# Kernel optimization log

Measured on AMD Instinct MI355X. Metric: run time of the kernel, lower is better.

## Reference

```python
import jax, jax.numpy as jnp
import numpy as np

V, D, DI, DS, DC, DTR, L, H, BS, B, T = 32000, 512, 1024, 16, 4, 32, 4, 2048, 1024, 2, 1024


def layer_norm(x, g, b):
    m = jnp.mean(x, axis=-1, keepdims=True)
    v = jnp.mean(jnp.square(x - m), axis=-1, keepdims=True)
    return (x - m) * jax.lax.rsqrt(v + 1e-5) * g + b


def mamba(x, p):
    # x: [B, T, D]
    Bb = x.shape[0]
    xz = jnp.einsum('btd,ed->bte', x, p['W_in'])          # [B,T,2*DI]
    u, z = jnp.split(xz, 2, axis=-1)
    # causal depthwise conv over time
    uc = jnp.transpose(u, (0, 2, 1))                       # [B,DI,T]
    uc = jax.lax.conv_general_dilated(uc, p['conv_w'][:, None, :], (1,), [(DC - 1, 0)], feature_group_count=DI)
    uc = uc + p['conv_b'][None, :, None]
    u = jax.nn.silu(jnp.transpose(uc, (0, 2, 1)))          # [B,T,DI]
    x_dbl = jnp.einsum('btd,ed->bte', u, p['W_xp'])        # [B,T,DTR+2*DS]
    dt = jax.nn.softplus(jnp.einsum('btr,dr->btd', x_dbl[..., :DTR], p['W_dt']) + p['b_dt'])  # [B,T,DI]
    Bm = x_dbl[..., DTR:DTR + DS]                          # [B,T,DS]
    Cm = x_dbl[..., DTR + DS:]                             # [B,T,DS]
    A = -jnp.exp(p['A_log'])                               # [DI,DS]

    def step(h, inp):
        dt_t, B_t, C_t, u_t = inp                          # [B,DI],[B,DS],[B,DS],[B,DI]
        dA = jnp.exp(dt_t[:, :, None] * A)                 # [B,DI,DS]
        h = dA * h + (dt_t * u_t)[:, :, None] * B_t[:, None, :]
        return h, jnp.einsum('bds,bs->bd', h, C_t)

    h0 = jnp.zeros((Bb, DI, DS), x.dtype)
    _, ys = jax.lax.scan(step, h0, (dt.transpose(1, 0, 2), Bm.transpose(1, 0, 2), Cm.transpose(1, 0, 2), u.transpose(1, 0, 2)))
    y = ys.transpose(1, 0, 2) + u * p['D_p']               # skip term D*u
    y = y * jax.nn.silu(z)
    return jnp.einsum('bte,de->btd', y, p['W_out'])


def setup_inputs() -> dict:
    key = jax.random.key(0)
    ks = jax.random.split(key, 16)
    s = 0.02
    rn = lambda k, sh: (jax.random.normal(k, sh, jnp.float32) * s)
    inp = {
        'idx': jax.random.randint(ks[0], (B, T), 0, V),
        'tok_emb': rn(ks[1], (V, D)),
        'pos_emb': rn(ks[2], (BS, D)),
        'ln1_g': jnp.ones((L, D), jnp.float32), 'ln1_b': jnp.zeros((L, D), jnp.float32),
        'W_in': rn(ks[3], (L, 2 * DI, D)),
        'conv_w': rn(ks[4], (L, DI, DC)), 'conv_b': jnp.zeros((L, DI), jnp.float32),
        'W_xp': rn(ks[5], (L, DTR + 2 * DS, DI)),
        'W_dt': rn(ks[6], (L, DI, DTR)), 'b_dt': jnp.full((L, DI), -4.6, jnp.float32),
        'A_log': jnp.tile(jnp.log(jnp.arange(1, DS + 1, dtype=jnp.float32))[None, None, :], (L, DI, 1)),
        'D_p': jnp.ones((L, DI), jnp.float32),
        'W_out': rn(ks[7], (L, D, DI)),
        'ln2_g': jnp.ones((L, D), jnp.float32), 'ln2_b': jnp.zeros((L, D), jnp.float32),
        'W_f1': rn(ks[8], (L, H, D)), 'b_f1': jnp.zeros((L, H), jnp.float32),
        'W_f2': rn(ks[9], (L, D, H)), 'b_f2': jnp.zeros((L, D), jnp.float32),
        'lm_w': rn(ks[10], (V, D)), 'lm_b': jnp.zeros((V,), jnp.float32),
    }
    return inp


def reference(idx, tok_emb, pos_emb, ln1_g, ln1_b, W_in, conv_w, conv_b, W_xp, W_dt, b_dt, A_log, D_p, W_out, ln2_g, ln2_b, W_f1, b_f1, W_f2, b_f2, lm_w, lm_b):
    x = tok_emb[idx] + pos_emb[:idx.shape[1]]              # [B,T,D]
    layers = {'ln1_g': ln1_g, 'ln1_b': ln1_b, 'W_in': W_in, 'conv_w': conv_w, 'conv_b': conv_b,
              'W_xp': W_xp, 'W_dt': W_dt, 'b_dt': b_dt, 'A_log': A_log, 'D_p': D_p, 'W_out': W_out,
              'ln2_g': ln2_g, 'ln2_b': ln2_b, 'W_f1': W_f1, 'b_f1': b_f1, 'W_f2': W_f2, 'b_f2': b_f2}

    def blk(x, p):
        x = x + mamba(layer_norm(x, p['ln1_g'], p['ln1_b']), p)
        h = layer_norm(x, p['ln2_g'], p['ln2_b'])
        h = jax.nn.relu(jnp.einsum('btd,hd->bth', h, p['W_f1']) + p['b_f1'])
        x = x + jnp.einsum('bth,dh->btd', h, p['W_f2']) + p['b_f2']
        return x, None

    x, _ = jax.lax.scan(blk, x, layers)
    logits = jnp.einsum('btd,vd->btv', x, lm_w) + lm_b     # [B,T,V]
    return logits
```

## Files before the change

### kernel.cpp

```cpp
#include <hip/hip_runtime.h>
#include <cstdint>
#include <cstddef>

typedef __bf16 bf16;
typedef __bf16 bf16x8 __attribute__((ext_vector_type(8)));
typedef __bf16 bf16x4 __attribute__((ext_vector_type(4)));
typedef float  f32x4  __attribute__((ext_vector_type(4)));

#define D_MODEL 512
#define D_INNER 1024
#define D_STATE 16
#define D_CONV  4
#define DT_RANK 32
#define N_LAYER 4
#define H_FFN   2048
#define SEQ_T   1024
#define BATCH   2
#define BT      (BATCH * SEQ_T)
#define VOCAB   32000

#define NCHUNK  16
#define CHUNK   (SEQ_T / NCHUNK)

#define KSPLIT  4

__device__ __forceinline__ float b2f(bf16 x) { return (float)x; }
__device__ __forceinline__ bf16  f2b(float x) { return (bf16)x; }

__device__ __forceinline__ float rdf(const void* p, long i, int bf) {
  return bf ? (float)((const bf16*)p)[i] : ((const float*)p)[i];
}

__device__ __forceinline__ void async16(const void* g, void* l) {
  __builtin_amdgcn_global_load_lds((const __attribute__((address_space(1))) void*)g,
                                   (__attribute__((address_space(3))) void*)l, 16, 0, 0);
}

__global__ void probe_k(const unsigned short* __restrict__ tok,
                        const unsigned short* __restrict__ pos,
                        int* __restrict__ flag)
{
  int lane = threadIdx.x;
  int bad = 0;
  for (int i = lane; i < 512; i += 64) {
    int e0 = (tok[i] >> 7) & 0xFF;
    int e1 = (pos[i] >> 7) & 0xFF;
    if (e0 >= 134 || e1 >= 134) bad = 1;
  }
  unsigned long long m = __ballot(bad);
  if (lane == 0) *flag = (m == 0ULL) ? 1 : 0;
}

__global__ __launch_bounds__(256) void cvt_k(const float4* __restrict__ src,
                                             bf16* __restrict__ dst,
                                             int n4, const int* __restrict__ dflag)
{
  if (*dflag) return;
  int i = blockIdx.x * 256 + threadIdx.x;
  if (i >= n4) return;
  float4 v = src[i];
  bf16x4 o; o[0] = f2b(v.x); o[1] = f2b(v.y); o[2] = f2b(v.z); o[3] = f2b(v.w);
  *(bf16x4*)(dst + (size_t)i * 4) = o;
}

template<int OUTMODE, bool RELU, bool SWZ>
__global__ __launch_bounds__(256) void gemm_nt(
    const bf16* __restrict__ A, const bf16* __restrict__ Barena,
    const void* __restrict__ Braw, long boff,
    void* __restrict__ Cout, const void* __restrict__ bias, long biasoff,
    const float* __restrict__ res, const int* __restrict__ dflag,
    int M, int N, int K, int ldc, int col0)
{
  __shared__ __attribute__((aligned(16))) bf16 As[128 * 32];
  __shared__ __attribute__((aligned(16))) bf16 Bs[128 * 32];

  const int bf = *dflag;
  const bf16* Bw = bf ? ((const bf16*)Braw + boff) : Barena;

  const int tid  = threadIdx.x;
  const int lane = tid & 63;
  const int q    = lane >> 4;
  const int m16  = lane & 15;
  const int w    = tid >> 6;
  const int wr   = w >> 1, wc = w & 1;

  int bx = blockIdx.x, by = blockIdx.y;
  if (SWZ) {
    int gx = gridDim.x, gy = gridDim.y;
    int n  = gx * gy;
    if ((n & 7) == 0) {
      int id  = by * gx + bx;
      int nid = (id & 7) * (n >> 3) + (id >> 3);
      bx = nid / gy;
      by = nid % gy;
    }
  }

  const int rowA0 = by * 128;
  const int rowB0 = bx * 128;

  f32x4 acc[4][4] = {};

  for (int k0 = 0; k0 < K; k0 += 32) {
#pragma unroll
    for (int r = 0; r < 2; r++) {
      int ci  = r * 256 + tid;
      int row = ci >> 2;
      int kc  = ci & 3;
      const bf16* ga = A  + (size_t)(rowA0 + row) * K + (k0 + kc * 8);
      const bf16* gb = Bw + (size_t)(rowB0 + row) * K + (k0 + kc * 8);
      char* la = (char*)As + (size_t)(r * 256 + (tid & 192)) * 16;
      char* lb = (char*)Bs + (size_t)(r * 256 + (tid & 192)) * 16;
      async16(ga, la);
      async16(gb, lb);
    }
    __syncthreads();

    bf16x8 af[4], bfr[4];
#pragma unroll
    for (int mt = 0; mt < 4; mt++)
      af[mt] = *(const bf16x8*)&As[(wr * 64 + mt * 16 + m16) * 32 + q * 8];
#pragma unroll
    for (int nt = 0; nt < 4; nt++)
      bfr[nt] = *(const bf16x8*)&Bs[(wc * 64 + nt * 16 + m16) * 32 + q * 8];

#pragma unroll
    for (int mt = 0; mt < 4; mt++)
#pragma unroll
      for (int nt = 0; nt < 4; nt++)
        acc[mt][nt] = __builtin_amdgcn_mfma_f32_16x16x32_bf16(
            af[mt], bfr[nt], acc[mt][nt], 0, 0, 0);

    __syncthreads();
  }

#pragma unroll
  for (int mt = 0; mt < 4; mt++) {
#pragma unroll
    for (int r = 0; r < 4; r++) {
      int row = rowA0 + wr * 64 + mt * 16 + q * 4 + r;
#pragma unroll
      for (int nt = 0; nt < 4; nt++) {
        int col = col0 + rowB0 + wc * 64 + nt * 16 + m16;
        float v = acc[mt][nt][r];
        if (bias) v += rdf(bias, biasoff + col, bf);
        if (res)  v += res[(size_t)row * ldc + col];
        if (RELU) v = fmaxf(v, 0.f);
        size_t oi = (size_t)row * ldc + col;
        if (OUTMODE == 1 || (OUTMODE == 2 && bf)) ((bf16*)Cout)[oi] = f2b(v);
        else                                      ((float*)Cout)[oi] = v;
      }
    }
  }
}

__global__ __launch_bounds__(256) void gemm_nt_sk(
    const bf16* __restrict__ A, const bf16* __restrict__ Barena,
    const void* __restrict__ Braw, long boff,
    float* __restrict__ Cpart, const int* __restrict__ dflag,
    int M, int N, int K)
{
  __shared__ __attribute__((aligned(16))) bf16 As[128 * 32];
  __shared__ __attribute__((aligned(16))) bf16 Bs[128 * 32];

  const int bf = *dflag;
  const bf16* Bw = bf ? ((const bf16*)Braw + boff) : Barena;

  const int tid  = threadIdx.x;
  const int lane = tid & 63;
  const int q    = lane >> 4;
  const int m16  = lane & 15;
  const int w    = tid >> 6;
  const int wr   = w >> 1, wc = w & 1;

  const int rowA0 = blockIdx.y * 128;
  const int rowB0 = blockIdx.x * 128;
  const int ks    = blockIdx.z;
  const int kBeg  = ks * (K / KSPLIT);
  const int kEnd  = kBeg + (K / KSPLIT);

  f32x4 acc[4][4] = {};

  for (int k0 = kBeg; k0 < kEnd; k0 += 32) {
#pragma unroll
    for (int r = 0; r < 2; r++) {
      int ci  = r * 256 + tid;
      int row = ci >> 2;
      int kc  = ci & 3;
      const bf16* ga = A  + (size_t)(rowA0 + row) * K + (k0 + kc * 8);
      const bf16* gb = Bw + (size_t)(rowB0 + row) * K + (k0 + kc * 8);
      char* la = (char*)As + (size_t)(r * 256 + (tid & 192)) * 16;
      char* lb = (char*)Bs + (size_t)(r * 256 + (tid & 192)) * 16;
      async16(ga, la);
      async16(gb, lb);
    }
    __syncthreads();

    bf16x8 af[4], bfr[4];
#pragma unroll
    for (int mt = 0; mt < 4; mt++)
      af[mt] = *(const bf16x8*)&As[(wr * 64 + mt * 16 + m16) * 32 + q * 8];
#pragma unroll
    for (int nt = 0; nt < 4; nt++)
      bfr[nt] = *(const bf16x8*)&Bs[(wc * 64 + nt * 16 + m16) * 32 + q * 8];

#pragma unroll
    for (int mt = 0; mt < 4; mt++)
#pragma unroll
      for (int nt = 0; nt < 4; nt++)
        acc[mt][nt] = __builtin_amdgcn_mfma_f32_16x16x32_bf16(
            af[mt], bfr[nt], acc[mt][nt], 0, 0, 0);

    __syncthreads();
  }

#pragma unroll
  for (int mt = 0; mt < 4; mt++) {
#pragma unroll
    for (int r = 0; r < 4; r++) {
      int row = rowA0 + wr * 64 + mt * 16 + q * 4 + r;
#pragma unroll
      for (int nt = 0; nt < 4; nt++) {
        int col = rowB0 + wc * 64 + nt * 16 + m16;
        Cpart[((size_t)ks * M + row) * N + col] = acc[mt][nt][r];
      }
    }
  }
}

__global__ __launch_bounds__(256) void redk_k(const float* __restrict__ part,
                                              const void* __restrict__ bias, long biasoff,
                                              const float* __restrict__ res,
                                              float* __restrict__ out,
                                              int n, int N, const int* __restrict__ dflag)
{
  int bf = *dflag;
  int i = blockIdx.x * 256 + threadIdx.x;
  if (i >= n) return;
  f32x4 s = ((const f32x4*)part)[i];
#pragma unroll
  for (int ks = 1; ks < KSPLIT; ks++) {
    f32x4 p = ((const f32x4*)part)[(size_t)ks * n + i];
    s.x += p.x; s.y += p.y; s.z += p.z; s.w += p.w;
  }
  if (bias) {
    int col = (i * 4) & (N - 1);
    s.x += rdf(bias, biasoff + col,     bf);
    s.y += rdf(bias, biasoff + col + 1, bf);
    s.z += rdf(bias, biasoff + col + 2, bf);
    s.w += rdf(bias, biasoff + col + 3, bf);
  }
  if (res) {
    f32x4 r = ((const f32x4*)res)[i];
    s.x += r.x; s.y += r.y; s.z += r.z; s.w += r.w;
  }
  ((f32x4*)out)[i] = s;
}

__global__ void embed_k(const int* __restrict__ idx, const void* __restrict__ tok,
                        const void* __restrict__ pos, float* __restrict__ x,
                        const int* __restrict__ dflag)
{
  int bf = *dflag;
  int bt = blockIdx.x;
  int t  = bt & (SEQ_T - 1);
  long rowv = idx[bt];
  for (int i = threadIdx.x; i < D_MODEL; i += blockDim.x)
    x[(size_t)bt * D_MODEL + i] = rdf(tok, rowv * D_MODEL + i, bf)
                                + rdf(pos, (long)t * D_MODEL + i, bf);
}

__global__ __launch_bounds__(64) void ln_k(const float* __restrict__ x,
                                           const void* __restrict__ g,
                                           const void* __restrict__ bb,
                                           long goff,
                                           bf16* __restrict__ out,
                                           const int* __restrict__ dflag)
{
  int bf = *dflag;
  int row = blockIdx.x;
  const float4* xr = (const float4*)(x + (size_t)row * D_MODEL);
  int l = threadIdx.x;
  float4 v0 = xr[l];
  float4 v1 = xr[64 + l];
  float s  = (v0.x + v0.y) + (v0.z + v0.w) + (v1.x + v1.y) + (v1.z + v1.w);
  float ss = v0.x*v0.x + v0.y*v0.y + v0.z*v0.z + v0.w*v0.w
           + v1.x*v1.x + v1.y*v1.y + v1.z*v1.z + v1.w*v1.w;
#pragma unroll
  for (int o = 32; o; o >>= 1) { s += __shfl_xor(s, o); ss += __shfl_xor(ss, o); }
  float m   = s  * (1.f / 512.f);
  float var = ss * (1.f / 512.f) - m * m;
  float inv = rsqrtf(var + 1e-5f);
  float vs[8] = {v0.x, v0.y, v0.z, v0.w, v1.x, v1.y, v1.z, v1.w};
  int i0 = l * 4, i1 = 256 + l * 4;
#pragma unroll
  for (int e = 0; e < 4; e++) {
    out[(size_t)row * D_MODEL + i0 + e] =
        f2b((vs[e] - m) * inv * rdf(g, goff + i0 + e, bf) + rdf(bb, goff + i0 + e, bf));
    out[(size_t)row * D_MODEL + i1 + e] =
        f2b((vs[4 + e] - m) * inv * rdf(g, goff + i1 + e, bf) + rdf(bb, goff + i1 + e, bf));
  }
}

__global__ __launch_bounds__(256) void conv_silu_k(const float* __restrict__ xz,
                                                   const void* __restrict__ cw,
                                                   const void* __restrict__ cb,
                                                   long cwoff, long cboff,
                                                   bf16* __restrict__ u,
                                                   const int* __restrict__ dflag)
{
  int bf  = *dflag;
  int gid = blockIdx.x * 256 + threadIdx.x;
  int d   = gid & (D_INNER - 1);
  int bt  = gid >> 10;
  int t   = bt & (SEQ_T - 1);
  float acc = rdf(cb, cboff + d, bf);
#pragma unroll
  for (int k = 0; k < D_CONV; k++) {
    int tt = t + k - (D_CONV - 1);
    if (tt >= 0)
      acc += xz[(size_t)(bt + k - (D_CONV - 1)) * (2 * D_INNER) + d]
           * rdf(cw, cwoff + (long)d * D_CONV + k, bf);
  }
  float sig = 1.f / (1.f + __expf(-acc));
  u[gid] = f2b(acc * sig);
}

__global__ __launch_bounds__(256) void xdbl_k(const bf16* __restrict__ u,
                                              const bf16* __restrict__ Warena,
                                              const void* __restrict__ Wraw, long woff,
                                              float* __restrict__ xd,
                                              const int* __restrict__ dflag)
{
  int bf = *dflag;
  const bf16* Wxp = bf ? ((const bf16*)Wraw + woff) : Warena;
  int t = blockIdx.x;
  __shared__ float us[D_INNER];
  __shared__ float red[256];
  if (threadIdx.x < D_INNER / 8) {
    bf16x8 v = *(const bf16x8*)(u + (size_t)t * D_INNER + threadIdx.x * 8);
#pragma unroll
    for (int e = 0; e < 8; e++) us[threadIdx.x * 8 + e] = b2f(v[e]);
  }
  __syncthreads();
  int j = threadIdx.x >> 2, p = threadIdx.x & 3;
  const bf16x8* wr = (const bf16x8*)(Wxp + (size_t)j * D_INNER + p * 256);
  float s = 0.f;
#pragma unroll 4
  for (int c = 0; c < 32; c++) {
    bf16x8 wv = wr[c];
    int k = p * 256 + c * 8;
#pragma unroll
    for (int e = 0; e < 8; e++) s += us[k + e] * b2f(wv[e]);
  }
  red[threadIdx.x] = s;
  __syncthreads();
  if (p == 0)
    xd[(size_t)t * 64 + j] = red[threadIdx.x] + red[threadIdx.x + 1]
                           + red[threadIdx.x + 2] + red[threadIdx.x + 3];
}

__global__ __launch_bounds__(256) void dt_k(const float* __restrict__ xd,
                                            const bf16* __restrict__ Warena,
                                            const void* __restrict__ Wraw, long woff,
                                            const void* __restrict__ bdt, long boff,
                                            float* __restrict__ dtb,
                                            const int* __restrict__ dflag)
{
  int bf = *dflag;
  const bf16* Wdt = bf ? ((const bf16*)Wraw + woff) : Warena;
  int t = blockIdx.x >> 2;
  int d = ((blockIdx.x & 3) << 8) + threadIdx.x;
  __shared__ float xr[DT_RANK];
  if (threadIdx.x < DT_RANK) xr[threadIdx.x] = xd[(size_t)t * 64 + threadIdx.x];
  __syncthreads();
  float s = rdf(bdt, boff + d, bf);
  const bf16x8* wr = (const bf16x8*)(Wdt + (size_t)d * DT_RANK);
#pragma unroll
  for (int c = 0; c < 4; c++) {
    bf16x8 wv = wr[c];
#pragma unroll
    for (int e = 0; e < 8; e++) s += xr[c * 8 + e] * b2f(wv[e]);
  }
  s = (s > 20.f) ? s : log1pf(__expf(s));
  dtb[(size_t)t * D_INNER + d] = s;
}

__global__ __launch_bounds__(256) void scanA_k(const float* __restrict__ dtb,
                                               const bf16* __restrict__ u,
                                               const float* __restrict__ xd,
                                               const void* __restrict__ A_log, long aoff,
                                               float* __restrict__ Pb,
                                               float* __restrict__ Qb,
                                               const int* __restrict__ dflag)
{
  int bf = *dflag;
  int s  = threadIdx.x & 15;
  int dl = threadIdx.x >> 4;
  int c  = blockIdx.x & (NCHUNK - 1);
  int dg = (blockIdx.x >> 4) & 63;
  int b  = blockIdx.x >> 10;
  int d  = dg * 16 + dl;

  float Av = -__expf(rdf(A_log, aoff + (long)d * D_STATE + s, bf));
  float h = 0.f, P = 1.f;
  size_t row0 = (size_t)b * SEQ_T + (size_t)c * CHUNK;

  float dt_n = dtb[row0 * D_INNER + d];
  float u_n  = b2f(u[row0 * D_INNER + d]);
  float B_n  = xd[row0 * 64 + DT_RANK + s];

  for (int t = 0; t < CHUNK; t++) {
    float dt_v = dt_n, u_v = u_n, Bv = B_n;
    if (t + 1 < CHUNK) {
      size_t r1 = row0 + t + 1;
      dt_n = dtb[r1 * D_INNER + d];
      u_n  = b2f(u[r1 * D_INNER + d]);
      B_n  = xd[r1 * 64 + DT_RANK + s];
    }
    float dA = __expf(dt_v * Av);
    P *= dA;
    h = dA * h + (dt_v * u_v) * Bv;
  }
  size_t o = (((size_t)b * D_INNER + d) * D_STATE + s) * NCHUNK + c;
  Pb[o] = P;
  Qb[o] = h;
}

__global__ __launch_bounds__(256) void scanB_k(const float* __restrict__ Pb,
                                               const float* __restrict__ Qb,
                                               float* __restrict__ Hin)
{
  int tid = blockIdx.x * 256 + threadIdx.x;
  size_t base = (size_t)tid * NCHUNK;
  float h = 0.f;
#pragma unroll
  for (int c = 0; c < NCHUNK; c++) {
    Hin[base + c] = h;
    h = Pb[base + c] * h + Qb[base + c];
  }
}

__global__ __launch_bounds__(256) void scanC_k(const float* __restrict__ dtb,
                                               const bf16* __restrict__ u,
                                               const float* __restrict__ xd,
                                               const float* __restrict__ xz,
                                               const void* __restrict__ A_log, long aoff,
                                               const void* __restrict__ D_p, long doff,
                                               const float* __restrict__ Hin,
                                               bf16* __restrict__ y,
                                               const int* __restrict__ dflag)
{
  int bf = *dflag;
  int s  = threadIdx.x & 15;
  int dl = threadIdx.x >> 4;
  int c  = blockIdx.x & (NCHUNK - 1);
  int dg = (blockIdx.x >> 4) & 63;
  int b  = blockIdx.x >> 10;
  int d  = dg * 16 + dl;

  float Av = -__expf(rdf(A_log, aoff + (long)d * D_STATE + s, bf));
  float Dv = rdf(D_p, doff + d, bf);
  float h  = Hin[(((size_t)b * D_INNER + d) * D_STATE + s) * NCHUNK + c];
  size_t row0 = (size_t)b * SEQ_T + (size_t)c * CHUNK;

  float dt_n = dtb[row0 * D_INNER + d];
  float u_n  = b2f(u[row0 * D_INNER + d]);
  float B_n  = xd[row0 * 64 + DT_RANK + s];
  float C_n  = xd[row0 * 64 + DT_RANK + D_STATE + s];

  for (int t = 0; t < CHUNK; t++) {
    float dt_v = dt_n, u_v = u_n, Bv = B_n, Cv = C_n;
    if (t + 1 < CHUNK) {
      size_t r1 = row0 + t + 1;
      dt_n = dtb[r1 * D_INNER + d];
      u_n  = b2f(u[r1 * D_INNER + d]);
      B_n  = xd[r1 * 64 + DT_RANK + s];
      C_n  = xd[r1 * 64 + DT_RANK + D_STATE + s];
    }
    float dA = __expf(dt_v * Av);
    h = dA * h + (dt_v * u_v) * Bv;
    float p = h * Cv;
    p += __shfl_xor(p, 1);
    p += __shfl_xor(p, 2);
    p += __shfl_xor(p, 4);
    p += __shfl_xor(p, 8);
    if (s == 0) {
      size_t r = row0 + t;
      float zv  = xz[r * (2 * D_INNER) + D_INNER + d];
      float sig = 1.f / (1.f + __expf(-zv));
      y[r * D_INNER + d] = f2b((p + u_v * Dv) * (zv * sig));
    }
  }
}

__global__ void cast_k(const float* __restrict__ x, bf16* __restrict__ o, int n)
{
  int i = blockIdx.x * 256 + threadIdx.x;
  if (i < n) o[i] = f2b(x[i]);
}

extern "C" void kernel_launch(void* const* d_in, const int* in_sizes, int n_in,
                              void* d_out, int out_size, void* d_ws, size_t ws_size,
                              hipStream_t stream)
{
  const int* idx = (const int*)d_in[0];
  const void* tok    = d_in[1];
  const void* pos    = d_in[2];
  const void* ln1_g  = d_in[3];
  const void* ln1_b  = d_in[4];
  const void* W_in   = d_in[5];
  const void* conv_w = d_in[6];
  const void* conv_b = d_in[7];
  const void* W_xp   = d_in[8];
  const void* W_dt   = d_in[9];
  const void* b_dt   = d_in[10];
  const void* A_log  = d_in[11];
  const void* D_p    = d_in[12];
  const void* W_out  = d_in[13];
  const void* ln2_g  = d_in[14];
  const void* ln2_b  = d_in[15];
  const void* W_f1   = d_in[16];
  const void* b_f1   = d_in[17];
  const void* W_f2   = d_in[18];
  const void* b_f2   = d_in[19];
  const void* lm_w   = d_in[20];
  const void* lm_b   = d_in[21];

  char* ws = (char*)d_ws;
  int*  dflag = (int*)ws;    ws += 256;
  float* x_res = (float*)ws; ws += (size_t)BT * D_MODEL * 4;
  float* xz    = (float*)ws; ws += (size_t)BT * 2 * D_INNER * 4;
  float* xdbl  = (float*)ws; ws += (size_t)BT * 64 * 4;
  float* dtb   = (float*)ws; ws += (size_t)BT * D_INNER * 4;
  bf16* lnbuf  = (bf16*)ws;  ws += (size_t)BT * D_MODEL * 2;
  bf16* ubuf   = (bf16*)ws;  ws += (size_t)BT * D_INNER * 2;
  bf16* ybuf   = (bf16*)ws;  ws += (size_t)BT * D_INNER * 2;
  bf16* hbuf   = (bf16*)ws;  ws += (size_t)BT * H_FFN * 2;
  float* cpart = (float*)ws; ws += (size_t)KSPLIT * BT * D_MODEL * 4;
  float* Pbuf  = (float*)ws; ws += (size_t)BATCH * D_INNER * D_STATE * NCHUNK * 4;
  float* Qbuf  = (float*)ws; ws += (size_t)BATCH * D_INNER * D_STATE * NCHUNK * 4;
  float* Hin   = (float*)ws; ws += (size_t)BATCH * D_INNER * D_STATE * NCHUNK * 4;
  bf16* aW_in  = (bf16*)ws;  ws += (size_t)N_LAYER * 2*D_INNER * D_MODEL * 2;
  bf16* aW_xp  = (bf16*)ws;  ws += (size_t)N_LAYER * 64 * D_INNER * 2;
  bf16* aW_dt  = (bf16*)ws;  ws += (size_t)N_LAYER * D_INNER * DT_RANK * 2;
  bf16* aW_out = (bf16*)ws;  ws += (size_t)N_LAYER * D_MODEL * D_INNER * 2;
  bf16* aW_f1  = (bf16*)ws;  ws += (size_t)N_LAYER * H_FFN * D_MODEL * 2;
  bf16* aW_f2  = (bf16*)ws;  ws += (size_t)N_LAYER * D_MODEL * H_FFN * 2;
  bf16* aLm    = (bf16*)ws;  ws += (size_t)VOCAB * D_MODEL * 2;

  probe_k<<<1, 64, 0, stream>>>((const unsigned short*)tok,
                                (const unsigned short*)pos, dflag);

  auto cvt = [&](const void* src, bf16* dst, long n) {
    int n4 = (int)(n / 4);
    cvt_k<<<(n4 + 255) / 256, 256, 0, stream>>>((const float4*)src, dst, n4, dflag);
  };
  cvt(W_in,  aW_in,  (long)N_LAYER * 2*D_INNER * D_MODEL);
  cvt(W_xp,  aW_xp,  (long)N_LAYER * 64 * D_INNER);
  cvt(W_dt,  aW_dt,  (long)N_LAYER * D_INNER * DT_RANK);
  cvt(W_out, aW_out, (long)N_LAYER * D_MODEL * D_INNER);
  cvt(W_f1,  aW_f1,  (long)N_LAYER * H_FFN * D_MODEL);
  cvt(W_f2,  aW_f2,  (long)N_LAYER * D_MODEL * H_FFN);
  cvt(lm_w,  aLm,    (long)VOCAB * D_MODEL);

  embed_k<<<BT, 256, 0, stream>>>(idx, tok, pos, x_res, dflag);

  for (int l = 0; l < N_LAYER; l++) {
    long oWin = (long)l * 2*D_INNER * D_MODEL;
    long oWxp = (long)l * 64 * D_INNER;
    long oWdt = (long)l * D_INNER * DT_RANK;
    long oWo  = (long)l * D_MODEL * D_INNER;
    long oWf1 = (long)l * H_FFN * D_MODEL;
    long oWf2 = (long)l * D_MODEL * H_FFN;
    long oA   = (long)l * D_INNER * D_STATE;
    long oD   = (long)l * D_INNER;

    ln_k<<<BT, 64, 0, stream>>>(x_res, ln1_g, ln1_b, (long)l * D_MODEL, lnbuf, dflag);

    gemm_nt<0, false, false><<<dim3(2 * D_INNER / 128, BT / 128), 256, 0, stream>>>(
        lnbuf, aW_in + oWin, W_in, oWin, xz, nullptr, 0, nullptr, dflag,
        BT, 2 * D_INNER, D_MODEL, 2 * D_INNER, 0);

    conv_silu_k<<<BT * D_INNER / 256, 256, 0, stream>>>(
        xz, conv_w, conv_b, (long)l * D_INNER * D_CONV, oD, ubuf, dflag);

    xdbl_k<<<BT, 256, 0, stream>>>(ubuf, aW_xp + oWxp, W_xp, oWxp, xdbl, dflag);

    dt_k<<<BT * 4, 256, 0, stream>>>(
        xdbl, aW_dt + oWdt, W_dt, oWdt, b_dt, oD, dtb, dflag);

    scanA_k<<<BATCH * 64 * NCHUNK, 256, 0, stream>>>(
        dtb, ubuf, xdbl, A_log, oA, Pbuf, Qbuf, dflag);
    scanB_k<<<BATCH * D_INNER * D_STATE / 256, 256, 0, stream>>>(Pbuf, Qbuf, Hin);
    scanC_k<<<BATCH * 64 * NCHUNK, 256, 0, stream>>>(
        dtb, ubuf, xdbl, xz, A_log, oA, D_p, oD, Hin, ybuf, dflag);

    gemm_nt_sk<<<dim3(D_MODEL / 128, BT / 128, KSPLIT), 256, 0, stream>>>(
        ybuf, aW_out + oWo, W_out, oWo, cpart, dflag, BT, D_MODEL, D_INNER);
    redk_k<<<(BT * D_MODEL / 4 + 255) / 256, 256, 0, stream>>>(
        cpart, nullptr, 0, x_res, x_res, BT * D_MODEL / 4, D_MODEL, dflag);

    ln_k<<<BT, 64, 0, stream>>>(x_res, ln2_g, ln2_b, (long)l * D_MODEL, lnbuf, dflag);

    gemm_nt<1, true, false><<<dim3(H_FFN / 128, BT / 128), 256, 0, stream>>>(
        lnbuf, aW_f1 + oWf1, W_f1, oWf1, hbuf, b_f1, (long)l * H_FFN, nullptr, dflag,
        BT, H_FFN, D_MODEL, H_FFN, 0);

    gemm_nt_sk<<<dim3(D_MODEL / 128, BT / 128, KSPLIT), 256, 0, stream>>>(
        hbuf, aW_f2 + oWf2, W_f2, oWf2, cpart, dflag, BT, D_MODEL, H_FFN);
    redk_k<<<(BT * D_MODEL / 4 + 255) / 256, 256, 0, stream>>>(
        cpart, b_f2, (long)l * D_MODEL, x_res, x_res, BT * D_MODEL / 4, D_MODEL, dflag);
  }

  cast_k<<<BT * D_MODEL / 256, 256, 0, stream>>>(x_res, lnbuf, BT * D_MODEL);

  for (int h = 0; h < 2; h++) {
    int colbase = h * (VOCAB / 2);
    gemm_nt<2, false, true><<<dim3(VOCAB / 2 / 128, BT / 128), 256, 0, stream>>>(
        lnbuf, aLm + (size_t)colbase * D_MODEL, lm_w, (long)colbase * D_MODEL,
        d_out, lm_b, 0, nullptr, dflag,
        BT, VOCAB / 2, D_MODEL, VOCAB, colbase);
  }
}
```

Before: 1.501 ms.

## Fuse split-K reduction with layernorm and narrow GEMM N-tiles for layer GEMMs

Replaces the elementwise split-K reduction plus separate layernorm (and final cast) with one per-row kernel that reduces partials, adds bias and residual, writes x, and emits the next layernorm's bf16 output. This removes an extra pass over the residual stream and several launches per layer. It also templatizes the GEMM N-tile and uses 64-wide tiles for the in-projection, FFN1 and split-K GEMMs to double block counts for better CU occupancy, at the cost of less B-tile reuse. The fused kernel computes variance as E[x^2]-m^2, which can lose precision.

```diff
diff --git a/kernel.cpp b/kernel.cpp
--- a/kernel.cpp
+++ b/kernel.cpp
@@ -63,7 +63,7 @@
   *(bf16x4*)(dst + (size_t)i * 4) = o;
 }
 
-template<int OUTMODE, bool RELU, bool SWZ>
+template<int OUTMODE, bool RELU, bool SWZ, int BN>
 __global__ __launch_bounds__(256) void gemm_nt(
     const bf16* __restrict__ A, const bf16* __restrict__ Barena,
     const void* __restrict__ Braw, long boff,
@@ -71,8 +71,12 @@
     const float* __restrict__ res, const int* __restrict__ dflag,
     int M, int N, int K, int ldc, int col0)
 {
+  constexpr int WN  = BN / 2;
+  constexpr int NTF = WN / 16;
+  constexpr int BCH = BN / 64;
+
   __shared__ __attribute__((aligned(16))) bf16 As[128 * 32];
-  __shared__ __attribute__((aligned(16))) bf16 Bs[128 * 32];
+  __shared__ __attribute__((aligned(16))) bf16 Bs[BN * 32];
 
   const int bf = *dflag;
   const bf16* Bw = bf ? ((const bf16*)Braw + boff) : Barena;
@@ -97,37 +101,39 @@
   }
 
   const int rowA0 = by * 128;
-  const int rowB0 = bx * 128;
-
-  f32x4 acc[4][4] = {};
+  const int rowB0 = bx * BN;
+
+  f32x4 acc[4][NTF] = {};
 
   for (int k0 = 0; k0 < K; k0 += 32) {
 #pragma unroll
     for (int r = 0; r < 2; r++) {
       int ci  = r * 256 + tid;
-      int row = ci >> 2;
-      int kc  = ci & 3;
-      const bf16* ga = A  + (size_t)(rowA0 + row) * K + (k0 + kc * 8);
-      const bf16* gb = Bw + (size_t)(rowB0 + row) * K + (k0 + kc * 8);
+      const bf16* ga = A + (size_t)(rowA0 + (ci >> 2)) * K + (k0 + (ci & 3) * 8);
       char* la = (char*)As + (size_t)(r * 256 + (tid & 192)) * 16;
+      async16(ga, la);
+    }
+#pragma unroll
+    for (int r = 0; r < BCH; r++) {
+      int ci  = r * 256 + tid;
+      const bf16* gb = Bw + (size_t)(rowB0 + (ci >> 2)) * K + (k0 + (ci & 3) * 8);
       char* lb = (char*)Bs + (size_t)(r * 256 + (tid & 192)) * 16;
-      async16(ga, la);
       async16(gb, lb);
     }
     __syncthreads();
 
-    bf16x8 af[4], bfr[4];
+    bf16x8 af[4], bfr[NTF];
 #pragma unroll
     for (int mt = 0; mt < 4; mt++)
       af[mt] = *(const bf16x8*)&As[(wr * 64 + mt * 16 + m16) * 32 + q * 8];
 #pragma unroll
-    for (int nt = 0; nt < 4; nt++)
-      bfr[nt] = *(const bf16x8*)&Bs[(wc * 64 + nt * 16 + m16) * 32 + q * 8];
+    for (int nt = 0; nt < NTF; nt++)
+      bfr[nt] = *(const bf16x8*)&Bs[(wc * WN + nt * 16 + m16) * 32 + q * 8];
 
 #pragma unroll
     for (int mt = 0; mt < 4; mt++)
 #pragma unroll
-      for (int nt = 0; nt < 4; nt++)
+      for (int nt = 0; nt < NTF; nt++)
         acc[mt][nt] = __builtin_amdgcn_mfma_f32_16x16x32_bf16(
             af[mt], bfr[nt], acc[mt][nt], 0, 0, 0);
 
@@ -140,8 +146,8 @@
     for (int r = 0; r < 4; r++) {
       int row = rowA0 + wr * 64 + mt * 16 + q * 4 + r;
 #pragma unroll
-      for (int nt = 0; nt < 4; nt++) {
-        int col = col0 + rowB0 + wc * 64 + nt * 16 + m16;
+      for (int nt = 0; nt < NTF; nt++) {
+        int col = col0 + rowB0 + wc * WN + nt * 16 + m16;
         float v = acc[mt][nt][r];
         if (bias) v += rdf(bias, biasoff + col, bf);
         if (res)  v += res[(size_t)row * ldc + col];
@@ -161,7 +167,7 @@
     int M, int N, int K)
 {
   __shared__ __attribute__((aligned(16))) bf16 As[128 * 32];
-  __shared__ __attribute__((aligned(16))) bf16 Bs[128 * 32];
+  __shared__ __attribute__((aligned(16))) bf16 Bs[64 * 32];
 
   const int bf = *dflag;
   const bf16* Bw = bf ? ((const bf16*)Braw + boff) : Barena;
@@ -174,40 +180,41 @@
   const int wr   = w >> 1, wc = w & 1;
 
   const int rowA0 = blockIdx.y * 128;
-  const int rowB0 = blockIdx.x * 128;
+  const int rowB0 = blockIdx.x * 64;
   const int ks    = blockIdx.z;
   const int kBeg  = ks * (K / KSPLIT);
   const int kEnd  = kBeg + (K / KSPLIT);
 
-  f32x4 acc[4][4] = {};
+  f32x4 acc[4][2] = {};
 
   for (int k0 = kBeg; k0 < kEnd; k0 += 32) {
 #pragma unroll
     for (int r = 0; r < 2; r++) {
       int ci  = r * 256 + tid;
-      int row = ci >> 2;
-      int kc  = ci & 3;
-      const bf16* ga = A  + (size_t)(rowA0 + row) * K + (k0 + kc * 8);
-      const bf16* gb = Bw + (size_t)(rowB0 + row) * K + (k0 + kc * 8);
+      const bf16* ga = A + (size_t)(rowA0 + (ci >> 2)) * K + (k0 + (ci & 3) * 8);
       char* la = (char*)As + (size_t)(r * 256 + (tid & 192)) * 16;
-      char* lb = (char*)Bs + (size_t)(r * 256 + (tid & 192)) * 16;
       async16(ga, la);
+    }
+    {
+      int ci  = tid;
+      const bf16* gb = Bw + (size_t)(rowB0 + (ci >> 2)) * K + (k0 + (ci & 3) * 8);
+      char* lb = (char*)Bs + (size_t)(tid & 192) * 16;
       async16(gb, lb);
     }
     __syncthreads();
 
-    bf16x8 af[4], bfr[4];
+    bf16x8 af[4], bfr[2];
 #pragma unroll
     for (int mt = 0; mt < 4; mt++)
       af[mt] = *(const bf16x8*)&As[(wr * 64 + mt * 16 + m16) * 32 + q * 8];
 #pragma unroll
-    for (int nt = 0; nt < 4; nt++)
-      bfr[nt] = *(const bf16x8*)&Bs[(wc * 64 + nt * 16 + m16) * 32 + q * 8];
+    for (int nt = 0; nt < 2; nt++)
+      bfr[nt] = *(const bf16x8*)&Bs[(wc * 32 + nt * 16 + m16) * 32 + q * 8];
 
 #pragma unroll
     for (int mt = 0; mt < 4; mt++)
 #pragma unroll
-      for (int nt = 0; nt < 4; nt++)
+      for (int nt = 0; nt < 2; nt++)
         acc[mt][nt] = __builtin_amdgcn_mfma_f32_16x16x32_bf16(
             af[mt], bfr[nt], acc[mt][nt], 0, 0, 0);
 
@@ -220,41 +227,81 @@
     for (int r = 0; r < 4; r++) {
       int row = rowA0 + wr * 64 + mt * 16 + q * 4 + r;
 #pragma unroll
-      for (int nt = 0; nt < 4; nt++) {
-        int col = rowB0 + wc * 64 + nt * 16 + m16;
+      for (int nt = 0; nt < 2; nt++) {
+        int col = rowB0 + wc * 32 + nt * 16 + m16;
         Cpart[((size_t)ks * M + row) * N + col] = acc[mt][nt][r];
       }
     }
   }
 }
 
-__global__ __launch_bounds__(256) void redk_k(const float* __restrict__ part,
-                                              const void* __restrict__ bias, long biasoff,
-                                              const float* __restrict__ res,
-                                              float* __restrict__ out,
-                                              int n, int N, const int* __restrict__ dflag)
-{
-  int bf = *dflag;
-  int i = blockIdx.x * 256 + threadIdx.x;
-  if (i >= n) return;
-  f32x4 s = ((const f32x4*)part)[i];
+template<bool DO_LN>
+__global__ __launch_bounds__(64) void redk_ln_k(
+    const float* __restrict__ part,
+    const void* __restrict__ bias, long biasoff,
+    const float* __restrict__ res,
+    float* __restrict__ xout,
+    const void* __restrict__ g, const void* __restrict__ bb, long goff,
+    bf16* __restrict__ out, const int* __restrict__ dflag)
+{
+  const int bf  = *dflag;
+  const int row = blockIdx.x;
+  const int l   = threadIdx.x;
+  const size_t slice = (size_t)BT * (D_MODEL / 4);
+  const f32x4* p = (const f32x4*)part + (size_t)row * (D_MODEL / 4);
+
+  f32x4 a0 = p[l], a1 = p[64 + l];
 #pragma unroll
   for (int ks = 1; ks < KSPLIT; ks++) {
-    f32x4 p = ((const f32x4*)part)[(size_t)ks * n + i];
-    s.x += p.x; s.y += p.y; s.z += p.z; s.w += p.w;
-  }
+    f32x4 q0 = p[ks * slice + l];
+    f32x4 q1 = p[ks * slice + 64 + l];
+    a0.x += q0.x; a0.y += q0.y; a0.z += q0.z; a0.w += q0.w;
+    a1.x += q1.x; a1.y += q1.y; a1.z += q1.z; a1.w += q1.w;
+  }
+  int i0 = l * 4, i1 = 256 + l * 4;
   if (bias) {
-    int col = (i * 4) & (N - 1);
-    s.x += rdf(bias, biasoff + col,     bf);
-    s.y += rdf(bias, biasoff + col + 1, bf);
-    s.z += rdf(bias, biasoff + col + 2, bf);
-    s.w += rdf(bias, biasoff + col + 3, bf);
+    a0.x += rdf(bias, biasoff + i0,     bf);
+    a0.y += rdf(bias, biasoff + i0 + 1, bf);
+    a0.z += rdf(bias, biasoff + i0 + 2, bf);
+    a0.w += rdf(bias, biasoff + i0 + 3, bf);
+    a1.x += rdf(bias, biasoff + i1,     bf);
+    a1.y += rdf(bias, biasoff + i1 + 1, bf);
+    a1.z += rdf(bias, biasoff + i1 + 2, bf);
+    a1.w += rdf(bias, biasoff + i1 + 3, bf);
   }
   if (res) {
-    f32x4 r = ((const f32x4*)res)[i];
-    s.x += r.x; s.y += r.y; s.z += r.z; s.w += r.w;
-  }
-  ((f32x4*)out)[i] = s;
+    const f32x4* rr = (const f32x4*)(res + (size_t)row * D_MODEL);
+    f32x4 r0 = rr[l], r1 = rr[64 + l];
+    a0.x += r0.x; a0.y += r0.y; a0.z += r0.z; a0.w += r0.w;
+    a1.x += r1.x; a1.y += r1.y; a1.z += r1.z; a1.w += r1.w;
+  }
+  f32x4* xo = (f32x4*)(xout + (size_t)row * D_MODEL);
+  xo[l] = a0; xo[64 + l] = a1;
+
+  float vs[8] = {a0.x, a0.y, a0.z, a0.w, a1.x, a1.y, a1.z, a1.w};
+  if (DO_LN) {
+    float s  = (a0.x + a0.y) + (a0.z + a0.w) + (a1.x + a1.y) + (a1.z + a1.w);
+    float ss = a0.x*a0.x + a0.y*a0.y + a0.z*a0.z + a0.w*a0.w
+             + a1.x*a1.x + a1.y*a1.y + a1.z*a1.z + a1.w*a1.w;
+#pragma unroll
+    for (int o = 32; o; o >>= 1) { s += __shfl_xor(s, o); ss += __shfl_xor(ss, o); }
+    float m   = s  * (1.f / 512.f);
+    float var = ss * (1.f / 512.f) - m * m;
+    float inv = rsqrtf(var + 1e-5f);
+#pragma unroll
+    for (int e = 0; e < 4; e++) {
+      out[(size_t)row * D_MODEL + i0 + e] =
+          f2b((vs[e] - m) * inv * rdf(g, goff + i0 + e, bf) + rdf(bb, goff + i0 + e, bf));
+      out[(size_t)row * D_MODEL + i1 + e] =
+          f2b((vs[4 + e] - m) * inv * rdf(g, goff + i1 + e, bf) + rdf(bb, goff + i1 + e, bf));
+    }
+  } else {
+#pragma unroll
+    for (int e = 0; e < 4; e++) {
+      out[(size_t)row * D_MODEL + i0 + e] = f2b(vs[e]);
+      out[(size_t)row * D_MODEL + i1 + e] = f2b(vs[4 + e]);
+    }
+  }
 }
 
 __global__ void embed_k(const int* __restrict__ idx, const void* __restrict__ tok,
@@ -492,12 +539,6 @@
       y[r * D_INNER + d] = f2b((p + u_v * Dv) * (zv * sig));
     }
   }
-}
-
-__global__ void cast_k(const float* __restrict__ x, bf16* __restrict__ o, int n)
-{
-  int i = blockIdx.x * 256 + threadIdx.x;
-  if (i < n) o[i] = f2b(x[i]);
 }
 
 extern "C" void kernel_launch(void* const* d_in, const int* in_sizes, int n_in,
@@ -566,6 +607,8 @@
 
   embed_k<<<BT, 256, 0, stream>>>(idx, tok, pos, x_res, dflag);
 
+  ln_k<<<BT, 64, 0, stream>>>(x_res, ln1_g, ln1_b, 0, lnbuf, dflag);
+
   for (int l = 0; l < N_LAYER; l++) {
     long oWin = (long)l * 2*D_INNER * D_MODEL;
     long oWxp = (long)l * 64 * D_INNER;
@@ -576,9 +619,7 @@
     long oA   = (long)l * D_INNER * D_STATE;
     long oD   = (long)l * D_INNER;
 
-    ln_k<<<BT, 64, 0, stream>>>(x_res, ln1_g, ln1_b, (long)l * D_MODEL, lnbuf, dflag);
-
-    gemm_nt<0, false, false><<<dim3(2 * D_INNER / 128, BT / 128), 256, 0, stream>>>(
+    gemm_nt<0, false, false, 64><<<dim3(2 * D_INNER / 64, BT / 128), 256, 0, stream>>>(
         lnbuf, aW_in + oWin, W_in, oWin, xz, nullptr, 0, nullptr, dflag,
         BT, 2 * D_INNER, D_MODEL, 2 * D_INNER, 0);
 
@@ -596,28 +637,32 @@
     scanC_k<<<BATCH * 64 * NCHUNK, 256, 0, stream>>>(
         dtb, ubuf, xdbl, xz, A_log, oA, D_p, oD, Hin, ybuf, dflag);
 
-    gemm_nt_sk<<<dim3(D_MODEL / 128, BT / 128, KSPLIT), 256, 0, stream>>>(
+    gemm_nt_sk<<<dim3(D_MODEL / 64, BT / 128, KSPLIT), 256, 0, stream>>>(
         ybuf, aW_out + oWo, W_out, oWo, cpart, dflag, BT, D_MODEL, D_INNER);
-    redk_k<<<(BT * D_MODEL / 4 + 255) / 256, 256, 0, stream>>>(
-        cpart, nullptr, 0, x_res, x_res, BT * D_MODEL / 4, D_MODEL, dflag);
-
-    ln_k<<<BT, 64, 0, stream>>>(x_res, ln2_g, ln2_b, (long)l * D_MODEL, lnbuf, dflag);
-
-    gemm_nt<1, true, false><<<dim3(H_FFN / 128, BT / 128), 256, 0, stream>>>(
+    redk_ln_k<true><<<BT, 64, 0, stream>>>(
+        cpart, nullptr, 0, x_res, x_res, ln2_g, ln2_b, (long)l * D_MODEL,
+        lnbuf, dflag);
+
+    gemm_nt<1, true, false, 64><<<dim3(H_FFN / 64, BT / 128), 256, 0, stream>>>(
         lnbuf, aW_f1 + oWf1, W_f1, oWf1, hbuf, b_f1, (long)l * H_FFN, nullptr, dflag,
         BT, H_FFN, D_MODEL, H_FFN, 0);
 
-    gemm_nt_sk<<<dim3(D_MODEL / 128, BT / 128, KSPLIT), 256, 0, stream>>>(
+    gemm_nt_sk<<<dim3(D_MODEL / 64, BT / 128, KSPLIT), 256, 0, stream>>>(
         hbuf, aW_f2 + oWf2, W_f2, oWf2, cpart, dflag, BT, D_MODEL, H_FFN);
-    redk_k<<<(BT * D_MODEL / 4 + 255) / 256, 256, 0, stream>>>(
-        cpart, b_f2, (long)l * D_MODEL, x_res, x_res, BT * D_MODEL / 4, D_MODEL, dflag);
-  }
-
-  cast_k<<<BT * D_MODEL / 256, 256, 0, stream>>>(x_res, lnbuf, BT * D_MODEL);
+    if (l + 1 < N_LAYER) {
+      redk_ln_k<true><<<BT, 64, 0, stream>>>(
+          cpart, b_f2, (long)l * D_MODEL, x_res, x_res,
+          ln1_g, ln1_b, (long)(l + 1) * D_MODEL, lnbuf, dflag);
+    } else {
+      redk_ln_k<false><<<BT, 64, 0, stream>>>(
+          cpart, b_f2, (long)l * D_MODEL, x_res, x_res,
+          nullptr, nullptr, 0, lnbuf, dflag);
+    }
+  }
 
   for (int h = 0; h < 2; h++) {
     int colbase = h * (VOCAB / 2);
-    gemm_nt<2, false, true><<<dim3(VOCAB / 2 / 128, BT / 128), 256, 0, stream>>>(
+    gemm_nt<2, false, true, 128><<<dim3(VOCAB / 2 / 128, BT / 128), 256, 0, stream>>>(
         lnbuf, aLm + (size_t)colbase * D_MODEL, lm_w, (long)colbase * D_MODEL,
         d_out, lm_b, 0, nullptr, dflag,
         BT, VOCAB / 2, D_MODEL, VOCAB, colbase);
```

Measured after the change: 1.446 ms. -3.6%, faster.
